# Optimization experiments

Hardware: AMD Instinct MI355X
Metric: run time of the kernel (lower is better)

## Reference

```python
import jax, jax.numpy as jnp
import numpy as np

N, D, E = 524288, 64, 4  # tokens, feature dim (d_in=64 default), num_expert=4


def setup_inputs() -> dict:
    key = jax.random.key(0)
    ks = jax.random.split(key, 5)
    s = 0.02
    return {
        "x": jax.random.normal(ks[0], (N, D), jnp.float32),
        "w_gate_a": jax.random.normal(ks[1], (D, E), jnp.float32) * s,
        "w_exp_a": jax.random.normal(ks[2], (E, D, D), jnp.float32) * s,
        "b_exp_a": jnp.zeros((E, D), jnp.float32),
        "w_gate_b": jax.random.normal(ks[3], (D, E), jnp.float32) * s,
        "w_exp_b": jax.random.normal(ks[4], (E, D, D), jnp.float32) * s,
        "b_exp_b": jnp.zeros((E, D), jnp.float32),
    }


def _moe_layer(x, w_gate, w_exp, b_exp):
    # Soft MoE: softmax gate over experts, each expert is (x - b_e) @ W_e.
    # Noise and PWLayer dropout are eval-mode identities.
    gates = jax.nn.softmax(x @ w_gate, axis=-1)            # [N, E]
    shifted = x[:, None, :] - b_exp[None, :, :]            # [N, E, D]
    expert_out = jnp.einsum('ned,edf->nef', shifted, w_exp)  # [N, E, D]
    return jnp.einsum('ne,nef->nf', gates, expert_out)     # [N, D]


def reference(x, w_gate_a, w_exp_a, b_exp_a, w_gate_b, w_exp_b, b_exp_b):
    residual = x
    h = _moe_layer(x, w_gate_a, w_exp_a, b_exp_a)
    # self.act is None (default) and nn.Dropout(0.5) is identity in eval mode
    h = _moe_layer(h, w_gate_b, w_exp_b, b_exp_b)
    return h + residual
```

## Files before the change

kernel.cpp:

```cpp
#include <hip/hip_runtime.h>
#include <math.h>


typedef __attribute__((ext_vector_type(8))) short short8;
typedef __attribute__((ext_vector_type(4))) short short4v;
typedef __attribute__((ext_vector_type(4))) float floatx4;

__device__ __forceinline__ float bf2f(unsigned short s) {
    unsigned int u = ((unsigned int)s) << 16;
    return __builtin_bit_cast(float, u);
}
__device__ __forceinline__ short f2bf(float f) {
    unsigned int u = __builtin_bit_cast(unsigned int, f);
    u += 0x7fffu + ((u >> 16) & 1u);
    return (short)(u >> 16);
}

#define NBLOCKS 512
#define TPW 4

__device__ __forceinline__ float ldf(const void* p, int isbf, int idx) {
    return isbf ? bf2f(((const unsigned short*)p)[idx]) : ((const float*)p)[idx];
}

__global__ __launch_bounds__(256, 2)
void moe2_fused(const void* __restrict__ x,
                const void* __restrict__ wg_a,
                const void* __restrict__ we_a,
                const void* __restrict__ be_a,
                const void* __restrict__ wg_b,
                const void* __restrict__ we_b,
                const void* __restrict__ be_b,
                void* __restrict__ outv)
{
    __shared__ alignas(16) short sB[2][17408];
    __shared__ float sC[2][4][64];
    __shared__ alignas(16) short sStage[4][1152];
    __shared__ int sBad[7];

    const int tid = threadIdx.x;

    const void* ps[7] = {x, wg_a, we_a, be_a, wg_b, we_b, be_b};
    if (tid < 7) sBad[tid] = 0;
    __syncthreads();
    if (tid < 64) {
        #pragma unroll
        for (int b = 0; b < 7; ++b) {
            const unsigned short s = ((const unsigned short*)ps[b])[2 * tid];
            const float a = fabsf(bf2f(s));
            const bool sane = (s == 0) || (a >= 9.3e-10f && a <= 1.1e9f);
            if (!sane) atomicAdd(&sBad[b], 1);
        }
    }
    __syncthreads();
    const int fx  = (sBad[0] < 16);
    const int fga = (sBad[1] < 16), fwa = (sBad[2] < 16), fba = (sBad[3] < 16);
    const int fgb = (sBad[4] < 16), fwb = (sBad[5] < 16), fbb = (sBad[6] < 16);

    for (int idx = tid; idx < 2 * 17 * 2 * 64; idx += 256) {
        const int L   = idx / 2176;
        const int rem = idx - L * 2176;
        const int t   = rem >> 7;
        const int kap = (rem >> 6) & 1;
        const int l2  = rem & 63;
        const int kb  = kap * 32 + (l2 >> 4) * 8;
        const int cc  = l2 & 15;
        const void* we = L ? we_b : we_a;
        const void* wg = L ? wg_b : wg_a;
        const int  fwe = L ? fwb : fwa;
        const int  fwg = L ? fgb : fga;
        short* dst = &sB[L][rem * 8];
        if (t < 16) {
            const int e = t >> 2;
            const int f = (t & 3) * 16 + cc;
            #pragma unroll
            for (int j = 0; j < 8; ++j)
                dst[j] = f2bf(ldf(we, fwe, (e * 64 + kb + j) * 64 + f));
        } else {
            #pragma unroll
            for (int j = 0; j < 8; ++j)
                dst[j] = (cc < 4) ? f2bf(ldf(wg, fwg, (kb + j) * 4 + cc)) : (short)0;
        }
    }
    for (int idx = tid; idx < 512; idx += 256) {
        const int L = idx >> 8;
        const int e = (idx >> 6) & 3;
        const int f = idx & 63;
        const void* we = L ? we_b : we_a;
        const void* be = L ? be_b : be_a;
        const int  fwe = L ? fwb : fwa;
        const int  fbe = L ? fbb : fba;
        float s = 0.f;
        for (int d = 0; d < 64; ++d)
            s += ldf(be, fbe, e * 64 + d) * ldf(we, fwe, (e * 64 + d) * 64 + f);
        sC[L][e][f] = s;
    }
    __syncthreads();

    const int l  = tid & 63;
    const int wv = tid >> 6;
    const int c  = l & 15;
    const int q  = l >> 4;
    short* stg = &sStage[wv][0];

    auto runLayer = [&](const short8 (&aF)[4][2], const int L, float (&acc)[4][4][4]) {
        const short* BL = &sB[L][0];
        floatx4 gA[4];
        {
            const short8 B0 = *(const short8*)&BL[(16 * 2 + 0) * 512 + l * 8];
            const short8 B1 = *(const short8*)&BL[(16 * 2 + 1) * 512 + l * 8];
            #pragma unroll
            for (int s = 0; s < 4; ++s) {
                floatx4 z = {0.f, 0.f, 0.f, 0.f};
                z = __builtin_amdgcn_mfma_f32_16x16x32_bf16(aF[s][0], B0, z, 0, 0, 0);
                z = __builtin_amdgcn_mfma_f32_16x16x32_bf16(aF[s][1], B1, z, 0, 0, 0);
                gA[s] = z;
            }
        }
        #pragma unroll
        for (int s = 0; s < 4; ++s) {
            float lg[4][4];
            #pragma unroll
            for (int e = 0; e < 4; ++e)
                #pragma unroll
                for (int r = 0; r < 4; ++r)
                    lg[e][r] = __shfl(gA[s][r], (l & 48) + e, 64);
            short gv[4];
            #pragma unroll
            for (int r = 0; r < 4; ++r) {
                const float m0 = fmaxf(fmaxf(lg[0][r], lg[1][r]), fmaxf(lg[2][r], lg[3][r]));
                const float e0 = __expf(lg[0][r] - m0);
                const float e1 = __expf(lg[1][r] - m0);
                const float e2 = __expf(lg[2][r] - m0);
                const float e3 = __expf(lg[3][r] - m0);
                const float inv = 1.f / (e0 + e1 + e2 + e3);
                const float mine = (c == 0) ? e0 : (c == 1) ? e1 : (c == 2) ? e2 : e3;
                gv[r] = f2bf(mine * inv);
            }
            if (c < 4) {
                short4v pk = {gv[0], gv[1], gv[2], gv[3]};
                *(short4v*)&stg[(s * 4 + c) * 16 + 4 * q] = pk;
            }
        }

        #pragma unroll
        for (int s = 0; s < 4; ++s)
            #pragma unroll
            for (int tt = 0; tt < 4; ++tt)
                #pragma unroll
                for (int r = 0; r < 4; ++r)
                    acc[s][tt][r] = 0.f;

        #pragma unroll
        for (int e = 0; e < 4; ++e) {
            float gse[4][4];
            #pragma unroll
            for (int s = 0; s < 4; ++s) {
                const short4v gp = *(const short4v*)&stg[(s * 4 + e) * 16 + 4 * q];
                #pragma unroll
                for (int r = 0; r < 4; ++r)
                    gse[s][r] = bf2f((unsigned short)gp[r]);
            }
            #pragma unroll
            for (int tt = 0; tt < 4; ++tt) {
                const int t = e * 4 + tt;
                const short8 B0 = *(const short8*)&BL[(t * 2 + 0) * 512 + l * 8];
                const short8 B1 = *(const short8*)&BL[(t * 2 + 1) * 512 + l * 8];
                const float ce = sC[L][e][tt * 16 + c];
                #pragma unroll
                for (int s = 0; s < 4; ++s) {
                    floatx4 z = {0.f, 0.f, 0.f, 0.f};
                    z = __builtin_amdgcn_mfma_f32_16x16x32_bf16(aF[s][0], B0, z, 0, 0, 0);
                    z = __builtin_amdgcn_mfma_f32_16x16x32_bf16(aF[s][1], B1, z, 0, 0, 0);
                    #pragma unroll
                    for (int r = 0; r < 4; ++r)
                        acc[s][tt][r] += gse[s][r] * (z[r] - ce);
                }
            }
        }
    };

    const int waveGlobal = blockIdx.x * 4 + wv;
    for (int it = 0; it < TPW; ++it) {
        const int tile = waveGlobal * TPW + it;
        const size_t tok0 = (size_t)tile * 64;

        short8 xF[4][2];
        if (fx) {
            const unsigned short* xu = (const unsigned short*)x;
            #pragma unroll
            for (int s = 0; s < 4; ++s)
                #pragma unroll
                for (int k = 0; k < 2; ++k)
                    xF[s][k] = *(const short8*)(xu + (tok0 + s * 16 + c) * 64 + k * 32 + q * 8);
        } else {
            const float* xf = (const float*)x;
            #pragma unroll
            for (int s = 0; s < 4; ++s)
                #pragma unroll
                for (int k = 0; k < 2; ++k) {
                    const float* xr = xf + (tok0 + s * 16 + c) * 64 + k * 32 + q * 8;
                    const floatx4 v0 = *(const floatx4*)xr;
                    const floatx4 v1 = *(const floatx4*)(xr + 4);
                    short8 f;
                    #pragma unroll
                    for (int j = 0; j < 4; ++j) { f[j] = f2bf(v0[j]); f[4 + j] = f2bf(v1[j]); }
                    xF[s][k] = f;
                }
        }

        float acc[4][4][4];
        runLayer(xF, 0, acc);

        short8 hF[4][2];
        #pragma unroll
        for (int s = 0; s < 4; ++s) {
            #pragma unroll
            for (int tt = 0; tt < 4; ++tt)
                #pragma unroll
                for (int r = 0; r < 4; ++r)
                    stg[(4 * q + r) * 72 + tt * 16 + c] = f2bf(acc[s][tt][r]);
            hF[s][0] = *(const short8*)&stg[c * 72 + 0 + q * 8];
            hF[s][1] = *(const short8*)&stg[c * 72 + 32 + q * 8];
        }

        runLayer(hF, 1, acc);

        if (fx) {
            unsigned short* ob = (unsigned short*)outv;
            #pragma unroll
            for (int s = 0; s < 4; ++s) {
                #pragma unroll
                for (int tt = 0; tt < 4; ++tt)
                    #pragma unroll
                    for (int r = 0; r < 4; ++r)
                        stg[(4 * q + r) * 72 + tt * 16 + c] = f2bf(acc[s][tt][r]);
                #pragma unroll
                for (int k = 0; k < 2; ++k) {
                    const short8 v = *(const short8*)&stg[c * 72 + k * 32 + q * 8];
                    short8 o;
                    #pragma unroll
                    for (int j = 0; j < 8; ++j)
                        o[j] = f2bf(bf2f((unsigned short)v[j]) + bf2f((unsigned short)xF[s][k][j]));
                    *(short8*)(ob + (tok0 + s * 16 + c) * 64 + k * 32 + q * 8) = o;
                }
            }
        } else {
            const float* xf = (const float*)x;
            float* of = (float*)outv;
            #pragma unroll
            for (int s = 0; s < 4; ++s)
                #pragma unroll
                for (int tt = 0; tt < 4; ++tt)
                    #pragma unroll
                    for (int r = 0; r < 4; ++r) {
                        const size_t o = (tok0 + s * 16 + 4 * q + r) * 64 + tt * 16 + c;
                        of[o] = acc[s][tt][r] + xf[o];
                    }
        }
    }
}

extern "C" void kernel_launch(void* const* d_in, const int* in_sizes, int n_in,
                              void* d_out, int out_size, void* d_ws, size_t ws_size,
                              hipStream_t stream) {
    hipLaunchKernelGGL(moe2_fused, dim3(NBLOCKS), dim3(256), 0, stream,
                       d_in[0], d_in[1], d_in[2], d_in[3], d_in[4], d_in[5], d_in[6],
                       d_out);
}
```

Baseline: 356.2 us.

## Use 1024-thread blocks and stage fp32 output through LDS for vector stores

Grows each block to 16 waves with 2 tiles per wave, so the shared weight setup is amortised over more work per block and fewer blocks are launched. The fp32 output path now transposes accumulators through a per-wave LDS scratch buffer, which allows coalesced float4 reads of the residual and float4 stores instead of scattered scalar accesses. The scratch buffer grows to float, which raises LDS use per block. The launch bound of 1024 threads may also cap registers per thread and cause spills.

```diff
diff --git a/kernel.cpp b/kernel.cpp
--- a/kernel.cpp
+++ b/kernel.cpp
@@ -16,14 +16,16 @@
     return (short)(u >> 16);
 }
 
-#define NBLOCKS 512
-#define TPW 4
+#define NBLOCKS 256
+#define NTHREADS 1024
+#define WPB 16
+#define TPW 2
 
 __device__ __forceinline__ float ldf(const void* p, int isbf, int idx) {
     return isbf ? bf2f(((const unsigned short*)p)[idx]) : ((const float*)p)[idx];
 }
 
-__global__ __launch_bounds__(256, 2)
+__global__ __launch_bounds__(NTHREADS, 4)
 void moe2_fused(const void* __restrict__ x,
                 const void* __restrict__ wg_a,
                 const void* __restrict__ we_a,
@@ -35,7 +37,7 @@
 {
     __shared__ alignas(16) short sB[2][17408];
     __shared__ float sC[2][4][64];
-    __shared__ alignas(16) short sStage[4][1152];
+    __shared__ alignas(16) float sScr[WPB][1088];
     __shared__ int sBad[7];
 
     const int tid = threadIdx.x;
@@ -57,7 +59,7 @@
     const int fga = (sBad[1] < 16), fwa = (sBad[2] < 16), fba = (sBad[3] < 16);
     const int fgb = (sBad[4] < 16), fwb = (sBad[5] < 16), fbb = (sBad[6] < 16);
 
-    for (int idx = tid; idx < 2 * 17 * 2 * 64; idx += 256) {
+    for (int idx = tid; idx < 2 * 17 * 2 * 64; idx += NTHREADS) {
         const int L   = idx / 2176;
         const int rem = idx - L * 2176;
         const int t   = rem >> 7;
@@ -82,7 +84,7 @@
                 dst[j] = (cc < 4) ? f2bf(ldf(wg, fwg, (kb + j) * 4 + cc)) : (short)0;
         }
     }
-    for (int idx = tid; idx < 512; idx += 256) {
+    for (int idx = tid; idx < 512; idx += NTHREADS) {
         const int L = idx >> 8;
         const int e = (idx >> 6) & 3;
         const int f = idx & 63;
@@ -101,7 +103,8 @@
     const int wv = tid >> 6;
     const int c  = l & 15;
     const int q  = l >> 4;
-    short* stg = &sStage[wv][0];
+    float* stf = &sScr[wv][0];
+    short* stg = (short*)stf;
 
     auto runLayer = [&](const short8 (&aF)[4][2], const int L, float (&acc)[4][4][4]) {
         const short* BL = &sB[L][0];
@@ -180,7 +183,7 @@
         }
     };
 
-    const int waveGlobal = blockIdx.x * 4 + wv;
+    const int waveGlobal = blockIdx.x * WPB + wv;
     for (int it = 0; it < TPW; ++it) {
         const int tile = waveGlobal * TPW + it;
         const size_t tok0 = (size_t)tile * 64;
@@ -249,14 +252,22 @@
             const float* xf = (const float*)x;
             float* of = (float*)outv;
             #pragma unroll
-            for (int s = 0; s < 4; ++s)
+            for (int s = 0; s < 4; ++s) {
                 #pragma unroll
                 for (int tt = 0; tt < 4; ++tt)
                     #pragma unroll
-                    for (int r = 0; r < 4; ++r) {
-                        const size_t o = (tok0 + s * 16 + 4 * q + r) * 64 + tt * 16 + c;
-                        of[o] = acc[s][tt][r] + xf[o];
-                    }
+                    for (int r = 0; r < 4; ++r)
+                        stf[(4 * q + r) * 68 + tt * 16 + c] = acc[s][tt][r];
+                const float* srcp = &stf[c * 68 + q * 16];
+                const size_t ro = (tok0 + s * 16 + c) * 64 + q * 16;
+                #pragma unroll
+                for (int jj = 0; jj < 4; ++jj) {
+                    const floatx4 v  = *(const floatx4*)(srcp + 4 * jj);
+                    const floatx4 xr = *(const floatx4*)(xf + ro + 4 * jj);
+                    const floatx4 o  = v + xr;
+                    *(floatx4*)(of + ro + 4 * jj) = o;
+                }
+            }
         }
     }
 }
@@ -264,7 +275,7 @@
 extern "C" void kernel_launch(void* const* d_in, const int* in_sizes, int n_in,
                               void* d_out, int out_size, void* d_ws, size_t ws_size,
                               hipStream_t stream) {
-    hipLaunchKernelGGL(moe2_fused, dim3(NBLOCKS), dim3(256), 0, stream,
+    hipLaunchKernelGGL(moe2_fused, dim3(NBLOCKS), dim3(NTHREADS), 0, stream,
                        d_in[0], d_in[1], d_in[2], d_in[3], d_in[4], d_in[5], d_in[6],
                        d_out);
 }
```

Result: slower. 438.5 us (+23.1%).
